# Performance work log

Measured on AMD Instinct MI355X. Metric: run time of the kernel, lower is better.

The kernel has to match this reference:

```python
import jax, jax.numpy as jnp
import numpy as np

B, S, D, H = 2, 2048, 1024, 16
DK = D // H  # 64


def setup_inputs() -> dict:
    key = jax.random.key(0)
    ks = jax.random.split(key, 7)
    sc = 1.0 / np.sqrt(D)  # lecun-normal-ish scaling for kernels
    return {
        "x_real": jax.random.normal(ks[0], (B, S, D), dtype=jnp.float32),
        "x_imag": jax.random.normal(ks[1], (B, S, D), dtype=jnp.float32),
        "Wq": jax.random.normal(ks[2], (D, D), dtype=jnp.float32) * sc,
        "bq": jnp.zeros((D,), dtype=jnp.float32),
        "Wk": jax.random.normal(ks[3], (D, D), dtype=jnp.float32) * sc,
        "bk": jnp.zeros((D,), dtype=jnp.float32),
        "Wv": jax.random.normal(ks[4], (D, D), dtype=jnp.float32) * sc,
        "bv": jnp.zeros((D,), dtype=jnp.float32),
        "Wo": jax.random.normal(ks[5], (D, D), dtype=jnp.float32) * sc,
        "bo": jnp.zeros((D,), dtype=jnp.float32),
    }


def reference(x_real, x_imag, Wq, bq, Wk, bk, Wv, bv, Wo, bo):
    cdt = jnp.complex64
    x = jax.lax.complex(x_real, x_imag)  # (B, S, D) complex64
    c = lambda w: w.astype(cdt)  # flax Dense(dtype=complex) casts real params

    def proj(W, b):
        # (B, S, D) -> (B, H, S, DK)
        y = jnp.einsum("bsd,de->bse", x, c(W)) + c(b)
        return y.reshape(B, S, H, DK).transpose(0, 2, 1, 3)

    Q = proj(Wq, bq)
    K = proj(Wk, bk)
    V = proj(Wv, bv)

    scale = jnp.sqrt(jnp.asarray(DK, dtype=cdt))
    scores = jnp.einsum("bhqd,bhkd->bhqk", Q, K) / scale  # complex (B,H,S,S)
    attn = jax.nn.softmax(scores.real, axis=-1).astype(cdt)  # softmax over real part
    out = jnp.einsum("bhqk,bhkd->bhqd", attn, V)  # (B, H, S, DK)
    out = out.transpose(0, 2, 1, 3).reshape(B, S, D)
    return jnp.einsum("bsd,de->bse", out, c(Wo)) + c(bo)
```

## Files before the change

### kernel.cpp

```cpp
#include <hip/hip_runtime.h>

#define NB 2
#define NS 2048
#define ND 1024
#define NH 16
#define NDK 64
#define NM (NB*NS)

typedef unsigned short u16;
typedef unsigned int u32;
typedef short bf16x8 __attribute__((ext_vector_type(8)));
typedef float f32x4 __attribute__((ext_vector_type(4)));
typedef const __attribute__((address_space(1))) void* gas_p;
typedef __attribute__((address_space(3))) void* las_p;

#define LOG2E 1.4426950408889634f
#define QSCALE (0.125f * LOG2E)

__device__ __forceinline__ u16 f2bf(float f) {
    unsigned u = __builtin_bit_cast(unsigned, f);
    u += 0x7fffu + ((u >> 16) & 1u);
    return (u16)(u >> 16);
}
__device__ __forceinline__ float bf2f(u16 h) {
    return __builtin_bit_cast(float, (unsigned)h << 16);
}
__device__ __forceinline__ u32 cvt_pk_bf16(float a, float b) {
    u32 r;
    asm("v_cvt_pk_bf16_f32 %0, %1, %2" : "=v"(r) : "v"(a), "v"(b));
    return r;
}

__global__ __launch_bounds__(256)
void conv_all(const float* __restrict__ xr, const float* __restrict__ xi,
              const float* __restrict__ W0, const float* __restrict__ W1,
              const float* __restrict__ W2, const float* __restrict__ W3,
              u16* __restrict__ XH, u16* __restrict__ WT)
{
    __shared__ float tls[64][68];
    const int tid = threadIdx.x;

    if (blockIdx.x < 8192) {
        const size_t gid = (size_t)blockIdx.x * 256 + tid;
        const size_t PQ = (size_t)NM * ND / 4;
        const int p = gid >= PQ;
        const size_t off = (gid - (p ? PQ : 0)) * 4;
        const float4 v = *(const float4*)&((p ? xi : xr)[off]);
        const size_t d = (size_t)p * NM * ND + off;
        float vs[4] = {v.x, v.y, v.z, v.w};
        ushort4 h;
        u16* hp = (u16*)&h;
        #pragma unroll
        for (int j = 0; j < 4; ++j) hp[j] = f2bf(vs[j]);
        *(ushort4*)&XH[d] = h;
        return;
    }

    const int bid2 = blockIdx.x - 8192;
    const int z = bid2 >> 8;
    const int rem = bid2 & 255;
    const int nt0 = (rem & 15) * 64;
    const int kt0 = ((rem >> 4) & 15) * 64;
    const float* W = z == 0 ? W0 : z == 1 ? W1 : z == 2 ? W2 : W3;
    u16* dh = WT + (size_t)z * 1048576;

    {
        const int kk = tid >> 4;
        const int nn = (tid & 15) * 4;
        #pragma unroll
        for (int i = 0; i < 4; ++i) {
            const float4 v = *(const float4*)&W[(size_t)(kt0 + kk + 16*i) * ND + nt0 + nn];
            tls[kk + 16*i][nn] = v.x; tls[kk + 16*i][nn+1] = v.y;
            tls[kk + 16*i][nn+2] = v.z; tls[kk + 16*i][nn+3] = v.w;
        }
    }
    __syncthreads();

    const int n  = tid >> 2;
    const int kc = (tid & 3) * 16;
    u16 hb[16];
    #pragma unroll
    for (int k = 0; k < 16; ++k) hb[k] = f2bf(tls[kc + k][n]);
    #pragma unroll
    for (int half = 0; half < 2; ++half)
        *(bf16x8*)&dh[(size_t)(nt0 + n) * ND + kt0 + kc + 8*half] = *(bf16x8*)&hb[8*half];
}

template<int MODE, int NTHR>
__global__ __launch_bounds__(NTHR)
void gemm_bf(const u16* __restrict__ Ah, const u16* __restrict__ Bh,
             const float* __restrict__ b0, const float* __restrict__ b1,
             const float* __restrict__ b2,
             u16* __restrict__ Qr_, u16* __restrict__ Qi_,
             u16* __restrict__ Kr_, u16* __restrict__ Ki_,
             u16* __restrict__ Vt_, float* __restrict__ Yf)
{
    constexpr int NW  = NTHR / 64;
    constexpr int CPW = 16 / NW;
    constexpr int FM  = (NTHR == 256) ? 4 : 2;
    constexpr int WROW = FM * 16;
    __shared__ u16 LDS[3][2][4096];

    const int tid  = threadIdx.x;
    const int wave = tid >> 6;
    const int lane = tid & 63;
    const int g = lane >> 4;
    const int c = lane & 15;
    const int wm = wave >> 1;
    const int wn = wave & 1;

    const int nbx = gridDim.x;
    const int nwg = nbx * gridDim.y;
    const int wgid = blockIdx.y * nbx + blockIdx.x;
    const int swz = (wgid & 7) * (nwg >> 3) + (wgid >> 3);
    const int row0 = (swz / nbx) * 128;
    const int col0 = (swz % nbx) * 128;

    if constexpr (MODE == 0) {
        if (col0 >= 2048 && row0 >= 4096) return;
    }

    const int lr = lane >> 2;
    const int lq = lane & 3;
    const u16* srcs[CPW];
    int doffs[CPW];
    #pragma unroll
    for (int i = 0; i < CPW; ++i) {
        const int ci = wave * CPW + i;
        const int p = ci >> 3;
        const int o = ci & 7;
        const u16* pl = p ? Bh : Ah;
        const int rb = p ? col0 : row0;
        srcs[i] = pl + (size_t)(rb + o*16 + lr) * ND + lq*8;
        doffs[i] = p*4096 + o*512;
    }

    f32x4 acc[FM][4];
    #pragma unroll
    for (int i = 0; i < FM; ++i)
        #pragma unroll
        for (int j = 0; j < 4; ++j)
            acc[i][j] = (f32x4){0.f, 0.f, 0.f, 0.f};

    #pragma unroll
    for (int i = 0; i < CPW; ++i)
        __builtin_amdgcn_global_load_lds((gas_p)srcs[i],
                                         (las_p)(&LDS[0][0][0] + doffs[i]), 16, 0, 0);
    #pragma unroll
    for (int i = 0; i < CPW; ++i)
        __builtin_amdgcn_global_load_lds((gas_p)(srcs[i] + 32),
                                         (las_p)(&LDS[1][0][0] + doffs[i]), 16, 0, 0);

    int cur = 0, nxt2 = 2;
    for (int t = 0; t < 32; ++t) {
        if (t < 30) {
            u16* ldst = &LDS[nxt2][0][0];
            #pragma unroll
            for (int i = 0; i < CPW; ++i)
                __builtin_amdgcn_global_load_lds((gas_p)(srcs[i] + (size_t)(t + 2) * 32),
                                                 (las_p)(ldst + doffs[i]), 16, 0, 0);
            if constexpr (CPW == 4) asm volatile("s_waitcnt vmcnt(8)" ::: "memory");
            else                    asm volatile("s_waitcnt vmcnt(4)" ::: "memory");
        } else if (t == 30) {
            if constexpr (CPW == 4) asm volatile("s_waitcnt vmcnt(4)" ::: "memory");
            else                    asm volatile("s_waitcnt vmcnt(2)" ::: "memory");
        } else {
            asm volatile("s_waitcnt vmcnt(0)" ::: "memory");
        }
        __builtin_amdgcn_sched_barrier(0);
        __builtin_amdgcn_s_barrier();
        __builtin_amdgcn_sched_barrier(0);

        const u16* AsH = &LDS[cur][0][0];
        const u16* BsH = &LDS[cur][1][0];

        bf16x8 a_h[FM], b_h[4];
        #pragma unroll
        for (int f = 0; f < FM; ++f)
            a_h[f] = *(const bf16x8*)&AsH[(wm*WROW + f*16 + c)*32 + 8*g];
        #pragma unroll
        for (int f = 0; f < 4; ++f)
            b_h[f] = *(const bf16x8*)&BsH[(wn*64 + f*16 + c)*32 + 8*g];

        __builtin_amdgcn_s_setprio(1);
        #pragma unroll
        for (int fm = 0; fm < FM; ++fm)
            #pragma unroll
            for (int fn = 0; fn < 4; ++fn)
                acc[fm][fn] = __builtin_amdgcn_mfma_f32_16x16x32_bf16(a_h[fm], b_h[fn], acc[fm][fn], 0, 0, 0);
        __builtin_amdgcn_s_setprio(0);
        __builtin_amdgcn_sched_barrier(0);
        __builtin_amdgcn_s_barrier();
        __builtin_amdgcn_sched_barrier(0);

        cur  = (cur  == 2) ? 0 : cur + 1;
        nxt2 = (nxt2 == 2) ? 0 : nxt2 + 1;
    }

    #pragma unroll
    for (int fm = 0; fm < FM; ++fm) {
        #pragma unroll
        for (int fn = 0; fn < 4; ++fn) {
            const int n = col0 + wn*64 + fn*16 + c;
            if constexpr (MODE == 0) {
                const int sel = n >> 10;
                const int nn = n & 1023;
                const int hh = nn >> 6;
                const int dk = nn & 63;
                if (sel == 2) {
                    const int m0 = row0 + wm*WROW + fm*16 + 4*g;
                    const int b  = m0 >> 11;
                    const int s  = m0 & (NS - 1);
                    const float bv = b2[nn];
                    uint2 pk;
                    pk.x = cvt_pk_bf16(acc[fm][fn][0] + bv, acc[fm][fn][1] + bv);
                    pk.y = cvt_pk_bf16(acc[fm][fn][2] + bv, acc[fm][fn][3] + bv);
                    *(uint2*)&Vt_[((size_t)(b*NH + hh) * NDK + dk) * NS + s] = pk;
                } else {
                    const float sc = sel ? 1.0f : QSCALE;
                    const float bb = (sel ? b1[nn] : b0[nn]) * sc;
                    #pragma unroll
                    for (int j = 0; j < 4; ++j) {
                        const int m = row0 + wm*WROW + fm*16 + 4*g + j;
                        const int plane = m >> 12;
                        const int mm = m & 4095;
                        const int b  = mm >> 11;
                        const int s  = mm & (NS - 1);
                        u16* dst = sel ? (plane ? Ki_ : Kr_) : (plane ? Qi_ : Qr_);
                        const float val = acc[fm][fn][j] * sc + (plane == 0 ? bb : 0.f);
                        dst[(((size_t)(b*NH + hh) * NS) + s) * NDK + dk] = f2bf(val);
                    }
                }
            } else {
                #pragma unroll
                for (int j = 0; j < 4; ++j) {
                    const int m = row0 + wm*WROW + fm*16 + 4*g + j;
                    Yf[(size_t)m * ND + n] = acc[fm][fn][j] + b0[n];
                }
            }
        }
    }
}

__global__ __launch_bounds__(512)
void attn_mfma(const u16* __restrict__ Qr, const u16* __restrict__ Qi,
               const u16* __restrict__ Kr, const u16* __restrict__ Ki,
               const u16* __restrict__ Vt, u16* __restrict__ OH)
{
    __shared__ __align__(16) u16 Ks[2][8192];
    __shared__ __align__(16) u16 Vs[2][2][4096];
    __shared__ __align__(16) u16 Ps[8][1024];

    const int tid  = threadIdx.x;
    const int wave = tid >> 6;
    const int lane = tid & 63;
    const int g = lane >> 4;
    const int c = lane & 15;

    const int nbx = gridDim.x;
    const int nwg = nbx * gridDim.y;
    const int wgid = blockIdx.y * nbx + blockIdx.x;
    const int swz = (wgid & 7) * (nwg >> 3) + (wgid >> 3);
    const int bh = swz / nbx;
    const int q0 = (swz % nbx) * 128;
    const size_t base = (size_t)bh * NS * NDK;

    bf16x8 qb[4];
    {
        const u16* qr = Qr + base + (size_t)(q0 + wave*16 + c) * NDK;
        const u16* qi = Qi + base + (size_t)(q0 + wave*16 + c) * NDK;
        #pragma unroll
        for (int s = 0; s < 2; ++s) {
            qb[s] = *(const bf16x8*)(qr + 32*s + 8*g);
            const bf16x8 t = *(const bf16x8*)(qi + 32*s + 8*g);
            bf16x8 f;
            #pragma unroll
            for (int j = 0; j < 8; ++j) f[j] = t[j] ^ (short)0x8000;
            qb[2+s] = f;
        }
    }

    const int slot = lane & 15;
    const int rloc = lane >> 4;
    const u16* kplane = (slot < 8 ? Kr : Ki) + base;
    const u16* srcK[2];
    #pragma unroll
    for (int i = 0; i < 2; ++i) {
        const int row = (wave*2 + i)*4 + rloc;
        srcK[i] = kplane + (size_t)row * NDK + ((slot ^ (row & 7)) & 7) * 8;
    }
    const int r8 = lane >> 3, sl = lane & 7;
    const int dkw = wave*8 + r8;
    const u16* srcV = Vt + base + (size_t)dkw * NS + ((sl ^ r8) & 7) * 8;

    const int swzmask = (c & 7) << 4;
    int offKa[4], offPa[2], offPw[4];
    #pragma unroll
    for (int s = 0; s < 4; ++s) offKa[s] = c*256 + ((64*s + 16*g) ^ swzmask);
    #pragma unroll
    for (int s = 0; s < 2; ++s) offPa[s] = wave*2048 + c*128 + ((64*s + 16*g) ^ swzmask);
    #pragma unroll
    for (int nt = 0; nt < 4; ++nt) offPw[nt] = wave*2048 + c*128 + ((32*nt + 8*g) ^ swzmask);
    const int oV0 = c*128 + ((16*g) ^ swzmask);
    const int oV1 = oV0 ^ 64;

    f32x4 oacc[4];
    #pragma unroll
    for (int nt = 0; nt < 4; ++nt) oacc[nt] = (f32x4){0.f, 0.f, 0.f, 0.f};
    float lrun = 0.f;

    #pragma unroll
    for (int h = 0; h < 2; ++h) {
        #pragma unroll
        for (int i = 0; i < 2; ++i)
            __builtin_amdgcn_global_load_lds((gas_p)(srcK[i] + (size_t)(h*64) * NDK),
                                             (las_p)(&Ks[h][0] + (wave*2 + i)*512), 16, 0, 0);
        __builtin_amdgcn_global_load_lds((gas_p)(srcV + h*64),
                                         (las_p)(&Vs[0][h][0] + wave*512), 16, 0, 0);
    }
    asm volatile("s_waitcnt vmcnt(0)" ::: "memory");
    __builtin_amdgcn_sched_barrier(0);
    __builtin_amdgcn_s_barrier();
    __builtin_amdgcn_sched_barrier(0);

    #define NTP (NS/128)
    for (int pt = 0; pt < NTP; ++pt) {
        const int cur = pt & 1;

        f32x4 sa[4], sb[4];
        #pragma unroll
        for (int nt = 0; nt < 4; ++nt) {
            sa[nt] = (f32x4){0.f, 0.f, 0.f, 0.f};
            sb[nt] = (f32x4){0.f, 0.f, 0.f, 0.f};
        }
        __builtin_amdgcn_s_setprio(1);
        #pragma unroll
        for (int s = 0; s < 4; ++s) {
            #pragma unroll
            for (int nt = 0; nt < 4; ++nt) {
                const bf16x8 ka = *(const bf16x8*)((const char*)&Ks[0][0] + offKa[s] + nt*4096);
                sa[nt] = __builtin_amdgcn_mfma_f32_16x16x32_bf16(ka, qb[s], sa[nt], 0, 0, 0);
            }
        }
        #pragma unroll
        for (int s = 0; s < 4; ++s) {
            #pragma unroll
            for (int nt = 0; nt < 4; ++nt) {
                const bf16x8 kb = *(const bf16x8*)((const char*)&Ks[0][0] + 16384 + offKa[s] + nt*4096);
                sb[nt] = __builtin_amdgcn_mfma_f32_16x16x32_bf16(kb, qb[s], sb[nt], 0, 0, 0);
            }
        }
        __builtin_amdgcn_s_setprio(0);
        __builtin_amdgcn_sched_barrier(0);
        __builtin_amdgcn_s_barrier();
        __builtin_amdgcn_sched_barrier(0);

        if (pt + 1 < NTP) {
            const int nk0 = (pt + 1) * 128;
            #pragma unroll
            for (int h = 0; h < 2; ++h) {
                #pragma unroll
                for (int i = 0; i < 2; ++i)
                    __builtin_amdgcn_global_load_lds((gas_p)(srcK[i] + (size_t)(nk0 + h*64) * NDK),
                                                     (las_p)(&Ks[h][0] + (wave*2 + i)*512), 16, 0, 0);
                __builtin_amdgcn_global_load_lds((gas_p)(srcV + nk0 + h*64),
                                                 (las_p)(&Vs[cur ^ 1][h][0] + wave*512), 16, 0, 0);
            }
        }

        #pragma unroll
        for (int nt = 0; nt < 4; ++nt) {
            float p0 = __builtin_amdgcn_exp2f(sa[nt][0]);
            float p1 = __builtin_amdgcn_exp2f(sa[nt][1]);
            float p2 = __builtin_amdgcn_exp2f(sa[nt][2]);
            float p3 = __builtin_amdgcn_exp2f(sa[nt][3]);
            lrun += (p0 + p1) + (p2 + p3);
            uint2 pk;
            pk.x = cvt_pk_bf16(p0, p1);
            pk.y = cvt_pk_bf16(p2, p3);
            *(uint2*)((char*)&Ps[0][0] + offPw[nt]) = pk;
        }
        {
            const int vbase = (cur*2 + 0) << 13;
            __builtin_amdgcn_s_setprio(1);
            #pragma unroll
            for (int s = 0; s < 2; ++s) {
                const bf16x8 pa = *(const bf16x8*)((const char*)&Ps[0][0] + offPa[s]);
                const int vbS = vbase + (s ? oV1 : oV0);
                #pragma unroll
                for (int nt = 0; nt < 4; ++nt) {
                    const bf16x8 vb = *(const bf16x8*)((const char*)&Vs[0][0][0] + vbS + nt*2048);
                    oacc[nt] = __builtin_amdgcn_mfma_f32_16x16x32_bf16(pa, vb, oacc[nt], 0, 0, 0);
                }
            }
            __builtin_amdgcn_s_setprio(0);
        }

        #pragma unroll
        for (int nt = 0; nt < 4; ++nt) {
            float p0 = __builtin_amdgcn_exp2f(sb[nt][0]);
            float p1 = __builtin_amdgcn_exp2f(sb[nt][1]);
            float p2 = __builtin_amdgcn_exp2f(sb[nt][2]);
            float p3 = __builtin_amdgcn_exp2f(sb[nt][3]);
            lrun += (p0 + p1) + (p2 + p3);
            uint2 pk;
            pk.x = cvt_pk_bf16(p0, p1);
            pk.y = cvt_pk_bf16(p2, p3);
            *(uint2*)((char*)&Ps[0][0] + offPw[nt]) = pk;
        }
        {
            const int vbase = (cur*2 + 1) << 13;
            __builtin_amdgcn_s_setprio(1);
            #pragma unroll
            for (int s = 0; s < 2; ++s) {
                const bf16x8 pa = *(const bf16x8*)((const char*)&Ps[0][0] + offPa[s]);
                const int vbS = vbase + (s ? oV1 : oV0);
                #pragma unroll
                for (int nt = 0; nt < 4; ++nt) {
                    const bf16x8 vb = *(const bf16x8*)((const char*)&Vs[0][0][0] + vbS + nt*2048);
                    oacc[nt] = __builtin_amdgcn_mfma_f32_16x16x32_bf16(pa, vb, oacc[nt], 0, 0, 0);
                }
            }
            __builtin_amdgcn_s_setprio(0);
        }

        if (pt + 1 < NTP) {
            asm volatile("s_waitcnt vmcnt(0)" ::: "memory");
            __builtin_amdgcn_sched_barrier(0);
            __builtin_amdgcn_s_barrier();
            __builtin_amdgcn_sched_barrier(0);
        }
    }

    lrun += __shfl_xor(lrun, 16, 64);
    lrun += __shfl_xor(lrun, 32, 64);
    const int b  = bh >> 4;
    const int hh = bh & 15;
    float linv[4];
    #pragma unroll
    for (int j = 0; j < 4; ++j) linv[j] = 1.0f / __shfl(lrun, 4*g + j, 64);
    #pragma unroll
    for (int j = 0; j < 4; ++j) {
        const int srow = q0 + wave*16 + 4*g + j;
        #pragma unroll
        for (int nt = 0; nt < 4; ++nt) {
            const size_t o = (size_t)(b*NS + srow)*ND + hh*NDK + nt*16 + c;
            OH[o] = f2bf(oacc[nt][j] * linv[j]);
        }
    }
}

extern "C" void kernel_launch(void* const* d_in, const int* in_sizes, int n_in,
                              void* d_out, int out_size, void* d_ws, size_t ws_size,
                              hipStream_t stream)
{
    const float* xr = (const float*)d_in[0];
    const float* xi = (const float*)d_in[1];
    const float* Wq = (const float*)d_in[2];
    const float* bq = (const float*)d_in[3];
    const float* Wk = (const float*)d_in[4];
    const float* bk = (const float*)d_in[5];
    const float* Wv = (const float*)d_in[6];
    const float* bv = (const float*)d_in[7];
    const float* Wo = (const float*)d_in[8];
    const float* bo = (const float*)d_in[9];
    float* out = (float*)d_out;

    u16* ws = (u16*)d_ws;
    const size_t PL = (size_t)NM * ND;
    u16* XH = ws;
    u16* WT = ws + 2*PL;
    u16* QP = WT + 4 * 1048576;
    u16* Qr = QP;          u16* Qi = QP + PL;
    u16* Kr = QP + 2*PL;   u16* Ki = QP + 3*PL;
    u16* Vt = QP + 4*PL;
    u16* OH = ws;

    conv_all<<<8192 + 1024, 256, 0, stream>>>(xr, xi, Wq, Wk, Wv, Wo, XH, WT);

    gemm_bf<0, 256><<<dim3(3*ND/128, 2*NM/128), 256, 0, stream>>>(
        XH, WT, bq, bk, bv, Qr, Qi, Kr, Ki, Vt, nullptr);

    attn_mfma<<<dim3(NS/128, NB*NH), 512, 0, stream>>>(Qr, Qi, Kr, Ki, Vt, OH);

    gemm_bf<1, 512><<<dim3(ND/128, NM/128), 512, 0, stream>>>(
        OH, WT + 3*1048576, bo, nullptr, nullptr,
        nullptr, nullptr, nullptr, nullptr, nullptr, out);
}
```

Measured before the change: 170.1 us.

## Process two K-tiles per barrier stage with double-buffered LDS pairs

```diff
diff --git a/kernel.cpp b/kernel.cpp
--- a/kernel.cpp
+++ b/kernel.cpp
@@ -99,7 +99,7 @@
     constexpr int CPW = 16 / NW;
     constexpr int FM  = (NTHR == 256) ? 4 : 2;
     constexpr int WROW = FM * 16;
-    __shared__ u16 LDS[3][2][4096];
+    __shared__ u16 LDS[4][2][4096];
 
     const int tid  = threadIdx.x;
     const int wave = tid >> 6;
@@ -143,27 +143,25 @@
             acc[i][j] = (f32x4){0.f, 0.f, 0.f, 0.f};
 
     #pragma unroll
-    for (int i = 0; i < CPW; ++i)
-        __builtin_amdgcn_global_load_lds((gas_p)srcs[i],
-                                         (las_p)(&LDS[0][0][0] + doffs[i]), 16, 0, 0);
-    #pragma unroll
-    for (int i = 0; i < CPW; ++i)
-        __builtin_amdgcn_global_load_lds((gas_p)(srcs[i] + 32),
-                                         (las_p)(&LDS[1][0][0] + doffs[i]), 16, 0, 0);
-
-    int cur = 0, nxt2 = 2;
-    for (int t = 0; t < 32; ++t) {
-        if (t < 30) {
-            u16* ldst = &LDS[nxt2][0][0];
-            #pragma unroll
-            for (int i = 0; i < CPW; ++i)
-                __builtin_amdgcn_global_load_lds((gas_p)(srcs[i] + (size_t)(t + 2) * 32),
-                                                 (las_p)(ldst + doffs[i]), 16, 0, 0);
+    for (int q = 0; q < 2; ++q)
+        #pragma unroll
+        for (int i = 0; i < CPW; ++i)
+            __builtin_amdgcn_global_load_lds((gas_p)(srcs[i] + (size_t)q * 32),
+                                             (las_p)(&LDS[q][0][0] + doffs[i]), 16, 0, 0);
+
+    for (int p = 0; p < 16; ++p) {
+        const int hb = (p & 1) * 2;
+        if (p < 15) {
+            const int nb = ((p + 1) & 1) * 2;
+            #pragma unroll
+            for (int q = 0; q < 2; ++q)
+                #pragma unroll
+                for (int i = 0; i < CPW; ++i)
+                    __builtin_amdgcn_global_load_lds(
+                        (gas_p)(srcs[i] + (size_t)(2*(p + 1) + q) * 32),
+                        (las_p)(&LDS[nb + q][0][0] + doffs[i]), 16, 0, 0);
             if constexpr (CPW == 4) asm volatile("s_waitcnt vmcnt(8)" ::: "memory");
             else                    asm volatile("s_waitcnt vmcnt(4)" ::: "memory");
-        } else if (t == 30) {
-            if constexpr (CPW == 4) asm volatile("s_waitcnt vmcnt(4)" ::: "memory");
-            else                    asm volatile("s_waitcnt vmcnt(2)" ::: "memory");
         } else {
             asm volatile("s_waitcnt vmcnt(0)" ::: "memory");
         }
@@ -171,30 +169,29 @@
         __builtin_amdgcn_s_barrier();
         __builtin_amdgcn_sched_barrier(0);
 
-        const u16* AsH = &LDS[cur][0][0];
-        const u16* BsH = &LDS[cur][1][0];
-
-        bf16x8 a_h[FM], b_h[4];
-        #pragma unroll
-        for (int f = 0; f < FM; ++f)
-            a_h[f] = *(const bf16x8*)&AsH[(wm*WROW + f*16 + c)*32 + 8*g];
-        #pragma unroll
-        for (int f = 0; f < 4; ++f)
-            b_h[f] = *(const bf16x8*)&BsH[(wn*64 + f*16 + c)*32 + 8*g];
-
-        __builtin_amdgcn_s_setprio(1);
-        #pragma unroll
-        for (int fm = 0; fm < FM; ++fm)
-            #pragma unroll
-            for (int fn = 0; fn < 4; ++fn)
-                acc[fm][fn] = __builtin_amdgcn_mfma_f32_16x16x32_bf16(a_h[fm], b_h[fn], acc[fm][fn], 0, 0, 0);
-        __builtin_amdgcn_s_setprio(0);
+        #pragma unroll
+        for (int q = 0; q < 2; ++q) {
+            const u16* AsH = &LDS[hb + q][0][0];
+            const u16* BsH = &LDS[hb + q][1][0];
+            bf16x8 a_h[FM], b_h[4];
+            #pragma unroll
+            for (int f = 0; f < FM; ++f)
+                a_h[f] = *(const bf16x8*)&AsH[(wm*WROW + f*16 + c)*32 + 8*g];
+            #pragma unroll
+            for (int f = 0; f < 4; ++f)
+                b_h[f] = *(const bf16x8*)&BsH[(wn*64 + f*16 + c)*32 + 8*g];
+
+            __builtin_amdgcn_s_setprio(1);
+            #pragma unroll
+            for (int fm = 0; fm < FM; ++fm)
+                #pragma unroll
+                for (int fn = 0; fn < 4; ++fn)
+                    acc[fm][fn] = __builtin_amdgcn_mfma_f32_16x16x32_bf16(a_h[fm], b_h[fn], acc[fm][fn], 0, 0, 0);
+            __builtin_amdgcn_s_setprio(0);
+        }
         __builtin_amdgcn_sched_barrier(0);
         __builtin_amdgcn_s_barrier();
         __builtin_amdgcn_sched_barrier(0);
-
-        cur  = (cur  == 2) ? 0 : cur + 1;
-        nxt2 = (nxt2 == 2) ? 0 : nxt2 + 1;
     }
 
     #pragma unroll
```

Measured after the change: 167.9 us. Within noise of the previous version (-1.3%).
